# Optimization experiments

Measured on AMD Instinct MI355X. Metric: run time of the kernel, lower is better.

## Reference

```python
import jax, jax.numpy as jnp
import numpy as np
from functools import partial

CONF_THR = 0.25
IOU_THR = 0.4
MAX_DET = 100
NMS_TOPK = 4096  # static candidate pool for JIT-safe NMS (>> MAX_DET)
N_ANCHORS = 120000
N_CLASSES = 80


def setup_inputs() -> dict:
    key = jax.random.key(0)
    k1, = jax.random.split(key, 1)
    # raw YOLOv5 head output: [1, N, 4(xywh) + 1(obj) + C(class probs)]
    prediction = jax.random.uniform(k1, (1, N_ANCHORS, 5 + N_CLASSES), dtype=jnp.float32)
    image_size = jnp.array([960, 1280], dtype=jnp.int64)  # original (h, w)
    input_size = jnp.array([480, 640], dtype=jnp.int64)   # network input (h, w)
    return {"prediction": prediction, "image_size": image_size, "input_size": input_size}


def _pairwise_iou(boxes):
    # boxes: [K, 4] xyxy -> [K, K] IoU
    x1, y1, x2, y2 = boxes[:, 0], boxes[:, 1], boxes[:, 2], boxes[:, 3]
    area = jnp.maximum(x2 - x1, 0.0) * jnp.maximum(y2 - y1, 0.0)
    ix1 = jnp.maximum(x1[:, None], x1[None, :])
    iy1 = jnp.maximum(y1[:, None], y1[None, :])
    ix2 = jnp.minimum(x2[:, None], x2[None, :])
    iy2 = jnp.minimum(y2[:, None], y2[None, :])
    inter = jnp.maximum(ix2 - ix1, 0.0) * jnp.maximum(iy2 - iy1, 0.0)
    union = area[:, None] + area[None, :] - inter
    return inter / jnp.maximum(union, 1e-9)


def _forward(prediction, image_size, input_size):
    det = prediction[0]                      # [N, 5+C]
    xy, wh = det[:, :2], det[:, 2:4]
    obj = det[:, 4]
    probs = det[:, 5:]                       # [N, C]
    clf = jnp.max(probs, axis=-1)
    labels = jnp.argmax(probs, axis=-1)
    scores = obj * clf
    boxes = jnp.concatenate([xy - wh * 0.5, xy + wh * 0.5], axis=-1)  # xywh -> xyxy

    valid = scores > CONF_THR
    masked_scores = jnp.where(valid, scores, -jnp.inf)
    # static top-K candidate pool, sorted by descending score (greedy NMS order)
    top_scores, top_idx = jax.lax.top_k(masked_scores, NMS_TOPK)
    cand_boxes = boxes[top_idx]              # [K, 4]
    cand_labels = labels[top_idx]
    cand_probs = probs[top_idx]              # [K, C]
    cand_valid = valid[top_idx]

    # class-batched NMS: offset boxes per class so boxes of different classes never overlap
    max_coord = jnp.max(jnp.where(cand_valid[:, None], cand_boxes, 0.0)) + 1.0
    off_boxes = cand_boxes + (cand_labels.astype(cand_boxes.dtype) * max_coord)[:, None]
    iou = _pairwise_iou(off_boxes)           # [K, K]

    K = NMS_TOPK
    idx = jnp.arange(K)

    def body(i, keep):
        suppress = keep[i] & (iou[i] > IOU_THR) & (idx > i)
        return keep & ~suppress

    keep = jax.lax.fori_loop(0, K, body, cand_valid)

    # take the MAX_DET highest-scoring kept boxes (candidates already score-sorted)
    sel_scores = jnp.where(keep, top_scores, -jnp.inf)
    fin_scores, fin_idx = jax.lax.top_k(sel_scores, MAX_DET)
    fin_valid = keep[fin_idx]
    fb = cand_boxes[fin_idx]                 # [MAX_DET, 4] xyxy, input-size coords
    fprobs = cand_probs[fin_idx]             # [MAX_DET, C]

    # rescale from input_size to image_size (undo letterbox), clip, then normalized xywh
    img = image_size.astype(fb.dtype)        # (h0, w0)
    inp = input_size.astype(fb.dtype)        # (h1, w1)
    gain = jnp.min(inp / img)
    pad = (inp - img * gain) * 0.5           # (pad_h, pad_w)
    x1 = jnp.clip((fb[:, 0] - pad[1]) / gain, 0.0, img[1])
    y1 = jnp.clip((fb[:, 1] - pad[0]) / gain, 0.0, img[0])
    x2 = jnp.clip((fb[:, 2] - pad[1]) / gain, 0.0, img[1])
    y2 = jnp.clip((fb[:, 3] - pad[0]) / gain, 0.0, img[0])
    h, w = img[0], img[1]
    out_boxes = jnp.stack([
        (x1 + x2) * 0.5 / w,
        (y1 + y2) * 0.5 / h,
        (x2 - x1) / w,
        (y2 - y1) / h,
    ], axis=-1)                               # [MAX_DET, 4]

    m = fin_valid.astype(out_boxes.dtype)[:, None]
    out_boxes = out_boxes * m                 # zero padded slots
    out_scores = jnp.where(fin_valid, fin_scores, 0.0)[:, None]
    out_probs = fprobs * m
    return out_boxes, out_scores, out_probs


def reference(prediction, image_size, input_size):
    return _forward(prediction, image_size, input_size)
```

## Files before the change

### kernel.cpp

```cpp
#include <hip/hip_runtime.h>
#include <math.h>

#define N_ANCH 120000
#define N_CLS  80
#define TOPK   4096
#define MAXDET 100
#define CONF   0.25f
#define IOUT   0.4f
#define KEYCAP 30720

__device__ __forceinline__ unsigned f2ord(float f) {
    unsigned u = __float_as_uint(f);
    return (u & 0x80000000u) ? ~u : (u | 0x80000000u);
}
__device__ __forceinline__ float ord2f(unsigned o) {
    unsigned u = (o & 0x80000000u) ? (o & 0x7FFFFFFFu) : ~o;
    return __uint_as_float(u);
}
__device__ __forceinline__ unsigned long long shflx64(unsigned long long v, int m) {
    unsigned lo = (unsigned)__shfl_xor((int)(unsigned)v, m, 64);
    unsigned hi = (unsigned)__shfl_xor((int)(unsigned)(v >> 32), m, 64);
    return ((unsigned long long)hi << 32) | lo;
}
#define ORD_NEGINF 0x007FFFFFu
#define BMAP(b) ((((b) & 0xFFu) << 8) | ((unsigned)(b) >> 8))

__global__ __launch_bounds__(256) void k_decode(const float* __restrict__ pred,
                                                unsigned* __restrict__ ord,
                                                int* __restrict__ lab,
                                                float4* __restrict__ box,
                                                unsigned* __restrict__ hist) {
    int wv = threadIdx.x >> 6, lane = threadIdx.x & 63;
    int a = blockIdx.x * 4 + wv;
    if (a >= N_ANCH) return;
    const float* p = pred + (long)a * 85;
    float v0 = p[lane];
    float v1 = (lane < 21) ? p[64 + lane] : 0.f;
    unsigned long long k0 = 0ull, k1 = 0ull;
    if (lane >= 5)
        k0 = ((unsigned long long)__float_as_uint(v0) << 32) | (0xFFFFFFFFu - (unsigned)(lane - 5));
    if (lane < 21)
        k1 = ((unsigned long long)__float_as_uint(v1) << 32) | (0xFFFFFFFFu - (unsigned)(59 + lane));
    unsigned long long key = k0 > k1 ? k0 : k1;
#pragma unroll
    for (int off = 1; off < 64; off <<= 1) {
        unsigned long long o = shflx64(key, off);
        if (o > key) key = o;
    }
    float best = __uint_as_float((unsigned)(key >> 32));
    int bl = (int)(0xFFFFFFFFu - (unsigned)(key & 0xFFFFFFFFu));
    float x = __shfl(v0, 0, 64), y = __shfl(v0, 1, 64);
    float w = __shfl(v0, 2, 64), h = __shfl(v0, 3, 64);
    float obj = __shfl(v0, 4, 64);
    if (lane == 0) {
        float sc = obj * best;
        bool valid = sc > CONF;
        float m = valid ? sc : -INFINITY;
        float hw = w * 0.5f, hh = h * 0.5f;
        float4 b;
        b.x = x - hw; b.y = y - hh; b.z = x + hw; b.w = y + hh;
        unsigned o = f2ord(m);
        ord[a] = o;
        lab[a] = bl;
        box[a] = b;
        if (valid) atomicAdd(&hist[BMAP(o >> 16)], 1u);
    }
}

__global__ __launch_bounds__(1024) void k_unpsel(const unsigned* __restrict__ hist,
                                                 unsigned* __restrict__ cnt,
                                                 unsigned* __restrict__ chunkSum,
                                                 unsigned* __restrict__ meta) {
    __shared__ unsigned part[1024];
    __shared__ bool isLast;
    int t = threadIdx.x;
    int b = blockIdx.x * 1024 + t;
    unsigned v = hist[BMAP(b)];
    cnt[b] = v;
    unsigned s = v;
#pragma unroll
    for (int off = 1; off < 64; off <<= 1) s += (unsigned)__shfl_xor((int)s, off, 64);
    if ((t & 63) == 0) chunkSum[b >> 6] = s;
    __syncthreads();
    if (t == 0) {
        __threadfence();
        unsigned done = atomicAdd(&meta[32], 1u);
        isLast = (done == 63u);
    }
    __syncthreads();
    if (!isLast) return;
    __threadfence();
    part[t] = chunkSum[t];
    __syncthreads();
    for (int off = 1; off < 1024; off <<= 1) {
        unsigned pv = (t + off < 1024) ? part[t + off] : 0u;
        __syncthreads();
        part[t] += pv;
        __syncthreads();
    }
    unsigned incl = part[t];
    unsigned after = (t + 1 < 1024) ? part[t + 1] : 0u;
    if (after < (unsigned)TOPK && incl >= (unsigned)TOPK) {
        int base = t * 64;
        unsigned c64[64];
#pragma unroll
        for (int i = 0; i < 64; ++i) c64[i] = cnt[base + i];
        unsigned run = after;
        for (int i = 63; i >= 0; --i) {
            unsigned c = c64[i];
            if (run + c >= (unsigned)TOPK) { meta[0] = (unsigned)(base + i); break; }
            run += c;
        }
    }
}

__global__ __launch_bounds__(256) void k_compact(const unsigned* __restrict__ ord,
                                                 unsigned* meta,
                                                 unsigned long long* __restrict__ keys) {
    __shared__ unsigned wc[4];
    __shared__ unsigned sBase;
    int a = blockIdx.x * 256 + threadIdx.x;
    int lane = threadIdx.x & 63, wv = threadIdx.x >> 6;
    unsigned b1 = meta[0];
    unsigned o = (a < N_ANCH) ? ord[a] : 0u;
    bool isC = (a < N_ANCH) && ((o >> 16) >= b1);
    unsigned long long bal = __ballot(isC);
    if (lane == 0) wc[wv] = (unsigned)__popcll(bal);
    __syncthreads();
    if (threadIdx.x == 0) {
        unsigned tg = wc[0] + wc[1] + wc[2] + wc[3];
        sBase = tg ? atomicAdd(&meta[6], tg) : 0u;
    }
    __syncthreads();
    unsigned long long ltmask = (lane == 63) ? ~0ull >> 1 : (1ull << lane) - 1ull;
    if (isC) {
        unsigned p = sBase;
        for (int w = 0; w < wv; ++w) p += wc[w];
        p += (unsigned)__popcll(bal & ltmask);
        if (p < KEYCAP) keys[p] = ((unsigned long long)o << 32) | (unsigned)(~(unsigned)a);
    }
}

__global__ __launch_bounds__(1024) void k_rank(const unsigned long long* __restrict__ keys,
                                               const int* __restrict__ lab,
                                               const float4* __restrict__ box,
                                               int* __restrict__ cIdx,
                                               float* __restrict__ cScore,
                                               int* __restrict__ cLab,
                                               float4* __restrict__ cBox,
                                               unsigned* meta) {
    __shared__ float smax[16];
    int wv = threadIdx.x >> 6, lane = threadIdx.x & 63;
    unsigned K = meta[6];
    if (K > KEYCAP) K = KEYCAP;
    int nw = (int)((K + 63) >> 6);
    float mymax = 0.f;
    for (int i = blockIdx.x * 16 + wv; i < (int)K; i += 256 * 16) {
        unsigned long long ki = keys[i];
        unsigned cnt = 0;
#pragma unroll 8
        for (int k = 0; k < nw; ++k) {
            int idx = (k << 6) + lane;
            unsigned long long kv = (idx < (int)K) ? keys[idx] : 0ull;
            cnt += (kv > ki) ? 1u : 0u;
        }
#pragma unroll
        for (int off = 1; off < 64; off <<= 1) cnt += (unsigned)__shfl_xor((int)cnt, off, 64);
        if (lane == 0 && cnt < (unsigned)TOPK) {
            int r = (int)cnt;
            unsigned o = (unsigned)(ki >> 32);
            unsigned a = ~(unsigned)(ki & 0xFFFFFFFFu);
            float sc = ord2f(o);
            cIdx[r] = (int)a;
            cScore[r] = sc;
            cLab[r] = lab[a];
            float4 b = box[a];
            cBox[r] = b;
            if (sc > CONF)
                mymax = fmaxf(mymax, fmaxf(0.f, fmaxf(fmaxf(b.x, b.y), fmaxf(b.z, b.w))));
        }
    }
    if (lane == 0) smax[wv] = mymax;
    __syncthreads();
    if (threadIdx.x == 0) {
        float m = 0.f;
#pragma unroll
        for (int q = 0; q < 16; ++q) m = fmaxf(m, smax[q]);
        if (m > 0.f) atomicMax(&meta[8], __float_as_uint(m));
    }
}

__global__ __launch_bounds__(256) void k_masknms(const float4* __restrict__ cBox,
                                                 const int* __restrict__ cLab,
                                                 unsigned* __restrict__ meta,
                                                 unsigned long long* __restrict__ M,
                                                 unsigned long long* __restrict__ Diag,
                                                 const float* __restrict__ cScore,
                                                 const int* __restrict__ cIdx,
                                                 const float* __restrict__ pred,
                                                 const int* __restrict__ img,
                                                 const int* __restrict__ inp,
                                                 float* __restrict__ out,
                                                 int out_size) {
    __shared__ unsigned long long keepW[64];
    __shared__ int sel[MAXDET];
    __shared__ int nsel;
    __shared__ bool isLast;
    int t = threadIdx.x;
    int lane = t & 63;
    {
        int i = blockIdx.x * 4 + (t >> 6);
        float mc = __uint_as_float(meta[8]) + 1.0f;
        float4 b = cBox[i];
        float offi = (float)cLab[i] * mc;
        float4 bi;
        bi.x = b.x + offi; bi.y = b.y + offi; bi.z = b.z + offi; bi.w = b.w + offi;
        float ai = fmaxf(bi.z - bi.x, 0.f) * fmaxf(bi.w - bi.y, 0.f);
        int w0 = i >> 6;
        unsigned long long myWord = 0ull;
        for (int jw = w0; jw < 64; ++jw) {
            int j = (jw << 6) + lane;
            float4 c = cBox[j];
            float offj = (float)cLab[j] * mc;
            float4 bj;
            bj.x = c.x + offj; bj.y = c.y + offj; bj.z = c.z + offj; bj.w = c.w + offj;
            float aj = fmaxf(bj.z - bj.x, 0.f) * fmaxf(bj.w - bj.y, 0.f);
            float ix1 = fmaxf(bi.x, bj.x), iy1 = fmaxf(bi.y, bj.y);
            float ix2 = fminf(bi.z, bj.z), iy2 = fminf(bi.w, bj.w);
            float inter = fmaxf(ix2 - ix1, 0.f) * fmaxf(iy2 - iy1, 0.f);
            float uni = ai + aj - inter;
            float iou = inter / fmaxf(uni, 1e-9f);
            bool bit = (j > i) & (iou > IOUT);
            unsigned long long word = __ballot(bit);
            if (lane == jw) myWord = word;
        }
        M[(long)i * 64 + lane] = myWord;
        if (lane == w0) Diag[i] = myWord;
    }
    __syncthreads();
    if (t == 0) {
        __threadfence();
        unsigned done = atomicAdd(&meta[33], 1u);
        isLast = (done == 1023u);
    }
    __syncthreads();
    if (!isLast) return;
    __threadfence();
    for (int i = t; i < out_size; i += 256) out[i] = 0.f;
    if (t == 0) nsel = 0;
    if (t < 64) {
        unsigned long long S = 0ull;
#pragma unroll 8
        for (int b = 0; b < 64; ++b) {
            float sc = cScore[(b << 6) + lane];
            unsigned long long bal = __ballot(!(sc > CONF));
            if (lane == b) S = bal;
        }
        unsigned long long d0 = Diag[lane];
        unsigned long long d1 = Diag[64 + lane];
        unsigned cntk = 0;
        int tstop = -1;
        unsigned long long ktStop = 0ull;
        for (int tt = 0; tt < 64; ++tt) {
            unsigned long long dcur = d0;
            d0 = d1;
            if (tt + 2 < 64) d1 = Diag[(tt + 2) * 64 + lane];
            unsigned long long s_tile =
                ((unsigned long long)(unsigned)__builtin_amdgcn_readlane((int)(unsigned)(S >> 32), tt)
                 << 32) |
                (unsigned)__builtin_amdgcn_readlane((int)(unsigned)S, tt);
#pragma unroll
            for (int b = 0; b < 64; ++b) {
                unsigned rl = (unsigned)__builtin_amdgcn_readlane((int)(unsigned)dcur, b);
                unsigned rh = (unsigned)__builtin_amdgcn_readlane((int)(unsigned)(dcur >> 32), b);
                unsigned long long row = ((unsigned long long)rh << 32) | rl;
                s_tile |= (((s_tile >> b) & 1ull) == 0ull) ? row : 0ull;
            }
            unsigned long long kt = ~s_tile;
            cntk += (unsigned)__popcll(kt);
            if (cntk >= MAXDET) { tstop = tt; ktStop = kt; break; }
            const unsigned long long* Mrow = M + (long)(tt << 6) * 64 + lane;
            unsigned long long a0 = 0, a1 = 0, a2 = 0, a3 = 0;
#pragma unroll
            for (int b = 0; b < 64; b += 4) {
                a0 |= Mrow[(long)(b + 0) * 64] & (0ull - ((kt >> (b + 0)) & 1ull));
                a1 |= Mrow[(long)(b + 1) * 64] & (0ull - ((kt >> (b + 1)) & 1ull));
                a2 |= Mrow[(long)(b + 2) * 64] & (0ull - ((kt >> (b + 2)) & 1ull));
                a3 |= Mrow[(long)(b + 3) * 64] & (0ull - ((kt >> (b + 3)) & 1ull));
            }
            S |= (a0 | a1) | (a2 | a3);
        }
        if (tstop >= 0) {
            keepW[lane] = (lane < tstop) ? ~S : (lane == tstop ? ktStop : 0ull);
        } else {
            keepW[lane] = ~S;
        }
    }
    __syncthreads();
    if (t < 64) {
        unsigned long long kw = keepW[t];
        int cntb = __popcll(kw);
        int incl = cntb;
        for (int off = 1; off < 64; off <<= 1) {
            int v = __shfl_up(incl, off);
            if (t >= off) incl += v;
        }
        int rk = incl - cntb;
        if (t == 63) nsel = (incl < MAXDET) ? incl : MAXDET;
        unsigned long long m = kw;
        while (m) {
            int b = __ffsll((unsigned long long)m) - 1;
            m &= m - 1;
            if (rk < MAXDET) sel[rk] = (t << 6) + b;
            ++rk;
        }
    }
    __syncthreads();
    int nk = nsel;
    int ih_i = img[0], iw_i = img[1];
    int nh_i = inp[0], nw_i = inp[1];
    if (iw_i == 0) iw_i = img[2];
    if (nw_i == 0) nw_i = inp[2];
    float ih = (float)ih_i, iw = (float)iw_i;
    float nh = (float)nh_i, nw = (float)nw_i;
    float gain = fminf(nh / ih, nw / iw);
    float pad0 = (nh - ih * gain) * 0.5f;
    float pad1 = (nw - iw * gain) * 0.5f;
    for (int o = t; o < nk; o += 256) {
        int k = sel[o];
        float4 b = cBox[k];
        float x1 = fminf(fmaxf((b.x - pad1) / gain, 0.f), iw);
        float y1 = fminf(fmaxf((b.y - pad0) / gain, 0.f), ih);
        float x2 = fminf(fmaxf((b.z - pad1) / gain, 0.f), iw);
        float y2 = fminf(fmaxf((b.w - pad0) / gain, 0.f), ih);
        out[o * 4 + 0] = (x1 + x2) * 0.5f / iw;
        out[o * 4 + 1] = (y1 + y2) * 0.5f / ih;
        out[o * 4 + 2] = (x2 - x1) / iw;
        out[o * 4 + 3] = (y2 - y1) / ih;
        out[4 * MAXDET + o] = cScore[k];
    }
    for (int p = t; p < nk * N_CLS; p += 256) {
        int o = p / N_CLS, c = p - o * N_CLS;
        int a = cIdx[sel[o]];
        out[5 * MAXDET + p] = pred[(long)a * 85 + 5 + c];
    }
}

extern "C" void kernel_launch(void* const* d_in, const int* in_sizes, int n_in,
                              void* d_out, int out_size, void* d_ws, size_t ws_size,
                              hipStream_t stream) {
    const float* pred = (const float*)d_in[0];
    const int* img = (const int*)d_in[1];
    const int* inp = (const int*)d_in[2];
    float* out = (float*)d_out;
    unsigned char* W = (unsigned char*)d_ws;

    unsigned* hist                = (unsigned*)(W + 0);
    unsigned* meta                = (unsigned*)(W + 262144);
    unsigned* ord                 = (unsigned*)(W + 262400);
    int* lab                      = (int*)(W + 742400);
    float4* box                   = (float4*)(W + 1222400);
    unsigned long long* keys      = (unsigned long long*)(W + 3142400);
    unsigned long long* M         = (unsigned long long*)(W + 3388160);
    unsigned long long* Diag      = (unsigned long long*)(W + 262400);
    int* cIdx                     = (int*)(W + 295168);
    float* cScore                 = (float*)(W + 311552);
    int* cLab                     = (int*)(W + 327936);
    float4* cBox                  = (float4*)(W + 344320);
    unsigned* cnt_lin             = (unsigned*)(W + 3388160);
    unsigned* chunkSum            = (unsigned*)(W + 3650304);

    hipMemsetAsync(W, 0, 262400, stream);

    int nb = (N_ANCH + 255) / 256;
    int nwb = (N_ANCH + 3) / 4;
    k_decode<<<nwb, 256, 0, stream>>>(pred, ord, lab, box, hist);
    k_unpsel<<<64, 1024, 0, stream>>>(hist, cnt_lin, chunkSum, meta);
    k_compact<<<nb, 256, 0, stream>>>(ord, meta, keys);
    k_rank<<<256, 1024, 0, stream>>>(keys, lab, box, cIdx, cScore, cLab, cBox, meta);
    k_masknms<<<1024, 256, 0, stream>>>(cBox, cLab, meta, M, Diag,
                                        cScore, cIdx, pred, img, inp, out, out_size);
}
```

Before: 136.9 us.

## Precompute IoU mask only for leading tiles; compute later tiles lazily in final NMS

Splits the fused mask+NMS kernel into a mask kernel that fills only the first 8 row-tiles of the suppression matrix, plus a single-block final kernel. For tiles beyond that, the final kernel computes diagonal and suppression IoU words on the fly and skips tiles after the MAX_DET stop. The last-block atomic handoff is replaced by a separate launch. This targets the cost of building the full 4096x4096 mask when greedy NMS usually stops early, but any tile past 8 now runs serially in one wave, and each kept row costs 64 IoUs per lane.

```diff
diff --git a/kernel.cpp b/kernel.cpp
--- a/kernel.cpp
+++ b/kernel.cpp
@@ -8,6 +8,7 @@
 #define CONF   0.25f
 #define IOUT   0.4f
 #define KEYCAP 30720
+#define PRETILES 8
 
 __device__ __forceinline__ unsigned f2ord(float f) {
     unsigned u = __float_as_uint(f);
@@ -24,6 +25,21 @@
 }
 #define ORD_NEGINF 0x007FFFFFu
 #define BMAP(b) ((((b) & 0xFFu) << 8) | ((unsigned)(b) >> 8))
+
+__device__ __forceinline__ void offbox(float4 c, int lb, float mc, float4* ob, float* ar) {
+    float off = (float)lb * mc;
+    float4 b;
+    b.x = c.x + off; b.y = c.y + off; b.z = c.z + off; b.w = c.w + off;
+    *ob = b;
+    *ar = fmaxf(b.z - b.x, 0.f) * fmaxf(b.w - b.y, 0.f);
+}
+__device__ __forceinline__ float ioU(float4 bi, float ai, float4 bj, float aj) {
+    float ix1 = fmaxf(bi.x, bj.x), iy1 = fmaxf(bi.y, bj.y);
+    float ix2 = fminf(bi.z, bj.z), iy2 = fminf(bi.w, bj.w);
+    float inter = fmaxf(ix2 - ix1, 0.f) * fmaxf(iy2 - iy1, 0.f);
+    float uni = ai + aj - inter;
+    return inter / fmaxf(uni, 1e-9f);
+}
 
 __global__ __launch_bounds__(256) void k_decode(const float* __restrict__ pred,
                                                 unsigned* __restrict__ ord,
@@ -190,65 +206,51 @@
     }
 }
 
-__global__ __launch_bounds__(256) void k_masknms(const float4* __restrict__ cBox,
-                                                 const int* __restrict__ cLab,
-                                                 unsigned* __restrict__ meta,
-                                                 unsigned long long* __restrict__ M,
-                                                 unsigned long long* __restrict__ Diag,
-                                                 const float* __restrict__ cScore,
-                                                 const int* __restrict__ cIdx,
-                                                 const float* __restrict__ pred,
-                                                 const int* __restrict__ img,
-                                                 const int* __restrict__ inp,
-                                                 float* __restrict__ out,
-                                                 int out_size) {
+__global__ __launch_bounds__(256) void k_mask(const float4* __restrict__ cBox,
+                                              const int* __restrict__ cLab,
+                                              const unsigned* __restrict__ meta,
+                                              unsigned long long* __restrict__ M,
+                                              unsigned long long* __restrict__ Diag) {
+    int lane = threadIdx.x & 63;
+    int i = blockIdx.x * 4 + (threadIdx.x >> 6);
+    float mc = __uint_as_float(meta[8]) + 1.0f;
+    float4 bi; float ai;
+    offbox(cBox[i], cLab[i], mc, &bi, &ai);
+    int w0 = i >> 6;
+    unsigned long long myWord = 0ull;
+    for (int jw = w0; jw < 64; ++jw) {
+        int j = (jw << 6) + lane;
+        float4 bj; float aj;
+        offbox(cBox[j], cLab[j], mc, &bj, &aj);
+        bool bit = (j > i) & (ioU(bi, ai, bj, aj) > IOUT);
+        unsigned long long word = __ballot(bit);
+        if (lane == jw) myWord = word;
+    }
+    M[(long)i * 64 + lane] = myWord;
+    if (lane == w0) Diag[i] = myWord;
+}
+
+__global__ __launch_bounds__(256) void k_nmsfinal(const unsigned long long* __restrict__ M,
+                                                  const unsigned long long* __restrict__ Diag,
+                                                  const float* __restrict__ cScore,
+                                                  const float4* __restrict__ cBox,
+                                                  const int* __restrict__ cLab,
+                                                  const int* __restrict__ cIdx,
+                                                  const unsigned* __restrict__ meta,
+                                                  const float* __restrict__ pred,
+                                                  const int* __restrict__ img,
+                                                  const int* __restrict__ inp,
+                                                  float* __restrict__ out,
+                                                  int out_size) {
     __shared__ unsigned long long keepW[64];
     __shared__ int sel[MAXDET];
     __shared__ int nsel;
-    __shared__ bool isLast;
     int t = threadIdx.x;
     int lane = t & 63;
-    {
-        int i = blockIdx.x * 4 + (t >> 6);
-        float mc = __uint_as_float(meta[8]) + 1.0f;
-        float4 b = cBox[i];
-        float offi = (float)cLab[i] * mc;
-        float4 bi;
-        bi.x = b.x + offi; bi.y = b.y + offi; bi.z = b.z + offi; bi.w = b.w + offi;
-        float ai = fmaxf(bi.z - bi.x, 0.f) * fmaxf(bi.w - bi.y, 0.f);
-        int w0 = i >> 6;
-        unsigned long long myWord = 0ull;
-        for (int jw = w0; jw < 64; ++jw) {
-            int j = (jw << 6) + lane;
-            float4 c = cBox[j];
-            float offj = (float)cLab[j] * mc;
-            float4 bj;
-            bj.x = c.x + offj; bj.y = c.y + offj; bj.z = c.z + offj; bj.w = c.w + offj;
-            float aj = fmaxf(bj.z - bj.x, 0.f) * fmaxf(bj.w - bj.y, 0.f);
-            float ix1 = fmaxf(bi.x, bj.x), iy1 = fmaxf(bi.y, bj.y);
-            float ix2 = fminf(bi.z, bj.z), iy2 = fminf(bi.w, bj.w);
-            float inter = fmaxf(ix2 - ix1, 0.f) * fmaxf(iy2 - iy1, 0.f);
-            float uni = ai + aj - inter;
-            float iou = inter / fmaxf(uni, 1e-9f);
-            bool bit = (j > i) & (iou > IOUT);
-            unsigned long long word = __ballot(bit);
-            if (lane == jw) myWord = word;
-        }
-        M[(long)i * 64 + lane] = myWord;
-        if (lane == w0) Diag[i] = myWord;
-    }
-    __syncthreads();
-    if (t == 0) {
-        __threadfence();
-        unsigned done = atomicAdd(&meta[33], 1u);
-        isLast = (done == 1023u);
-    }
-    __syncthreads();
-    if (!isLast) return;
-    __threadfence();
     for (int i = t; i < out_size; i += 256) out[i] = 0.f;
     if (t == 0) nsel = 0;
     if (t < 64) {
+        float mc = __uint_as_float(meta[8]) + 1.0f;
         unsigned long long S = 0ull;
 #pragma unroll 8
         for (int b = 0; b < 64; ++b) {
@@ -256,15 +258,27 @@
             unsigned long long bal = __ballot(!(sc > CONF));
             if (lane == b) S = bal;
         }
-        unsigned long long d0 = Diag[lane];
-        unsigned long long d1 = Diag[64 + lane];
         unsigned cntk = 0;
         int tstop = -1;
         unsigned long long ktStop = 0ull;
         for (int tt = 0; tt < 64; ++tt) {
-            unsigned long long dcur = d0;
-            d0 = d1;
-            if (tt + 2 < 64) d1 = Diag[(tt + 2) * 64 + lane];
+            unsigned long long dcur;
+            if (tt < PRETILES) {
+                dcur = Diag[(tt << 6) + lane];
+            } else {
+                int j = (tt << 6) + lane;
+                float4 bj; float aj;
+                offbox(cBox[j], cLab[j], mc, &bj, &aj);
+                dcur = 0ull;
+                for (int r = 0; r < 64; ++r) {
+                    int i = (tt << 6) + r;
+                    float4 bi; float ai;
+                    offbox(cBox[i], cLab[i], mc, &bi, &ai);
+                    bool bit = (j > i) & (ioU(bi, ai, bj, aj) > IOUT);
+                    unsigned long long word = __ballot(bit);
+                    if (lane == r) dcur = word;
+                }
+            }
             unsigned long long s_tile =
                 ((unsigned long long)(unsigned)__builtin_amdgcn_readlane((int)(unsigned)(S >> 32), tt)
                  << 32) |
@@ -279,16 +293,36 @@
             unsigned long long kt = ~s_tile;
             cntk += (unsigned)__popcll(kt);
             if (cntk >= MAXDET) { tstop = tt; ktStop = kt; break; }
-            const unsigned long long* Mrow = M + (long)(tt << 6) * 64 + lane;
-            unsigned long long a0 = 0, a1 = 0, a2 = 0, a3 = 0;
-#pragma unroll
-            for (int b = 0; b < 64; b += 4) {
-                a0 |= Mrow[(long)(b + 0) * 64] & (0ull - ((kt >> (b + 0)) & 1ull));
-                a1 |= Mrow[(long)(b + 1) * 64] & (0ull - ((kt >> (b + 1)) & 1ull));
-                a2 |= Mrow[(long)(b + 2) * 64] & (0ull - ((kt >> (b + 2)) & 1ull));
-                a3 |= Mrow[(long)(b + 3) * 64] & (0ull - ((kt >> (b + 3)) & 1ull));
+            if (tt < PRETILES) {
+                const unsigned long long* Mrow = M + (long)(tt << 6) * 64 + lane;
+                unsigned long long a0 = 0, a1 = 0, a2 = 0, a3 = 0;
+#pragma unroll
+                for (int b = 0; b < 64; b += 4) {
+                    a0 |= Mrow[(long)(b + 0) * 64] & (0ull - ((kt >> (b + 0)) & 1ull));
+                    a1 |= Mrow[(long)(b + 1) * 64] & (0ull - ((kt >> (b + 1)) & 1ull));
+                    a2 |= Mrow[(long)(b + 2) * 64] & (0ull - ((kt >> (b + 2)) & 1ull));
+                    a3 |= Mrow[(long)(b + 3) * 64] & (0ull - ((kt >> (b + 3)) & 1ull));
+                }
+                S |= (a0 | a1) | (a2 | a3);
+            } else {
+                unsigned long long acc = 0ull;
+                for (int b = 0; b < 64; ++b) {
+                    if (!((kt >> b) & 1ull)) continue;
+                    int i = (tt << 6) + b;
+                    float4 bi; float ai;
+                    offbox(cBox[i], cLab[i], mc, &bi, &ai);
+                    unsigned long long w = 0ull;
+                    for (int c2 = 0; c2 < 64; ++c2) {
+                        int j = (lane << 6) + c2;
+                        float4 bj; float aj;
+                        offbox(cBox[j], cLab[j], mc, &bj, &aj);
+                        bool bit = (j > i) & (ioU(bi, ai, bj, aj) > IOUT);
+                        w |= ((unsigned long long)(bit ? 1 : 0)) << c2;
+                    }
+                    acc |= w;
+                }
+                S |= acc;
             }
-            S |= (a0 | a1) | (a2 | a3);
         }
         if (tstop >= 0) {
             keepW[lane] = (lane < tstop) ? ~S : (lane == tstop ? ktStop : 0ull);
@@ -378,6 +412,7 @@
     k_unpsel<<<64, 1024, 0, stream>>>(hist, cnt_lin, chunkSum, meta);
     k_compact<<<nb, 256, 0, stream>>>(ord, meta, keys);
     k_rank<<<256, 1024, 0, stream>>>(keys, lab, box, cIdx, cScore, cLab, cBox, meta);
-    k_masknms<<<1024, 256, 0, stream>>>(cBox, cLab, meta, M, Diag,
-                                        cScore, cIdx, pred, img, inp, out, out_size);
-}
+    k_mask<<<PRETILES * 16, 256, 0, stream>>>(cBox, cLab, meta, M, Diag);
+    k_nmsfinal<<<1, 256, 0, stream>>>(M, Diag, cScore, cBox, cLab, cIdx, meta,
+                                      pred, img, inp, out, out_size);
+}
```

New measurement: 128.7 us. -6.0%, faster.
